# Kernel optimization log

Measured on AMD Instinct MI355X. Metric: run time of the kernel, lower is better.

The kernel has to match this reference:

```python
import jax, jax.numpy as jnp
import numpy as np

D, NH, NL, NP, DFF = 256, 8, 4, 4, 1024
DH = D // NH
SHAPES = [(64, 64), (32, 32), (16, 16), (8, 8)]
LEN = sum(h * w for h, w in SHAPES)  # 5440
B = 4
EPS = 1e-5


def setup_inputs() -> dict:
    key = jax.random.key(0)
    ks = jax.random.split(key, 24)
    def lin_w(k, fin, fout, scale=None):
        s = (1.0 / np.sqrt(fin)) if scale is None else scale
        return jax.random.normal(k, (fin, fout), jnp.float32) * s
    def lin_b(k, fout, scale=0.01):
        return jax.random.normal(k, (fout,), jnp.float32) * scale
    inp = {
        'src': jax.random.normal(ks[0], (B, LEN, D), jnp.float32),
        'pos_lvl_embed': jax.random.normal(ks[1], (B, LEN, D), jnp.float32),
        'spatial_shapes': jnp.array(SHAPES, jnp.int32),
        'level_start_index': jnp.array(np.cumsum([0] + [h * w for h, w in SHAPES[:-1]]), jnp.int32),
        # MSDeformAttn params
        'Wv': lin_w(ks[2], D, D), 'bv': lin_b(ks[3], D),
        'Woff': lin_w(ks[4], D, NH * NL * NP * 2, scale=0.001),  # small offsets, like grid init
        'boff': jax.random.normal(ks[5], (NH * NL * NP * 2,), jnp.float32) * 0.5,
        'Wa': lin_w(ks[6], D, NH * NL * NP), 'ba': lin_b(ks[7], NH * NL * NP),
        'Wo': lin_w(ks[8], D, D), 'bo': lin_b(ks[9], D),
        # FFN params
        'W1': lin_w(ks[10], D, DFF), 'b1': lin_b(ks[11], DFF),
        'W2': lin_w(ks[12], DFF, D), 'b2': lin_b(ks[13], D),
        # LayerNorms
        'g1': jnp.ones((D,), jnp.float32), 'be1': jnp.zeros((D,), jnp.float32),
        'g2': jnp.ones((D,), jnp.float32), 'be2': jnp.zeros((D,), jnp.float32),
    }
    return inp


def _layernorm(x, g, b):
    mu = jnp.mean(x, axis=-1, keepdims=True)
    var = jnp.var(x, axis=-1, keepdims=True)
    return (x - mu) * jax.lax.rsqrt(var + EPS) * g + b


def _bilinear(v, x, y):
    # v: [B, H, W, NH, DH]; x, y: [B, Lq, NH, NP] pixel coords (align_corners=False, zero padding)
    Bv, H, W = v.shape[0], v.shape[1], v.shape[2]
    x0, y0 = jnp.floor(x), jnp.floor(y)
    bb = jnp.arange(Bv)[:, None, None, None]
    hh = jnp.arange(NH)[None, None, :, None]
    out = 0.0
    for dx in (0, 1):
        for dy in (0, 1):
            xi, yi = x0 + dx, y0 + dy
            w = (1.0 - jnp.abs(x - xi)) * (1.0 - jnp.abs(y - yi))
            valid = (xi >= 0) & (xi <= W - 1) & (yi >= 0) & (yi <= H - 1)
            xc = jnp.clip(xi, 0, W - 1).astype(jnp.int32)
            yc = jnp.clip(yi, 0, H - 1).astype(jnp.int32)
            out = out + v[bb, yc, xc, hh] * (w * valid)[..., None]
    return out  # [B, Lq, NH, NP, DH]


def _ms_deform_attn(query, value_flat, shapes, starts, Wv, bv, Woff, boff, Wa, ba, Wo, bo):
    Bq, Lq = query.shape[0], query.shape[1]
    # reference points: normalized center of each query's own spatial location (valid_ratios == 1)
    refs = []
    for (H, W) in shapes:
        gy, gx = jnp.meshgrid(jnp.arange(H, dtype=jnp.float32), jnp.arange(W, dtype=jnp.float32), indexing='ij')
        refs.append(jnp.stack([(gx + 0.5) / W, (gy + 0.5) / H], -1).reshape(-1, 2))
    ref = jnp.concatenate(refs, 0)  # [Len, 2] (x, y)

    value = (value_flat @ Wv + bv).reshape(Bq, Lq, NH, DH)
    off = (query @ Woff + boff).reshape(Bq, Lq, NH, NL, NP, 2)
    attn = jax.nn.softmax((query @ Wa + ba).reshape(Bq, Lq, NH, NL * NP), axis=-1).reshape(Bq, Lq, NH, NL, NP)
    norm = jnp.array([[w, h] for (h, w) in shapes], jnp.float32)  # [NL, 2] = (W, H)
    loc = ref[None, :, None, None, None, :] + off / norm[None, None, None, :, None, :]  # [B,Lq,NH,NL,NP,2]

    out = 0.0
    for l, (H, W) in enumerate(shapes):
        s = starts[l]
        v_l = value[:, s:s + H * W].reshape(Bq, H, W, NH, DH)
        x = loc[:, :, :, l, :, 0] * W - 0.5
        y = loc[:, :, :, l, :, 1] * H - 0.5
        sampled = _bilinear(v_l, x, y)  # [B,Lq,NH,NP,DH]
        out = out + jnp.sum(sampled * attn[:, :, :, l, :, None], axis=3)
    return out.reshape(Bq, Lq, D) @ Wo + bo


def reference(src, spatial_shapes, level_start_index, pos_lvl_embed,
              Wv, bv, Woff, boff, Wa, ba, Wo, bo,
              W1, b1, W2, b2, g1, be1, g2, be2):
    shapes = [(int(h), int(w)) for h, w in np.asarray(spatial_shapes)]  # static metadata
    starts = [int(s) for s in np.asarray(level_start_index)]
    src2 = _ms_deform_attn(src + pos_lvl_embed, src, shapes, starts, Wv, bv, Woff, boff, Wa, ba, Wo, bo)
    x = _layernorm(src + src2, g1, be1)
    ffn = jax.nn.relu(x @ W1 + b1) @ W2 + b2
    return _layernorm(x + ffn, g2, be2)
```

## Files before the change

### kernel.cpp

```cpp
#include <hip/hip_runtime.h>
#include <hip/hip_fp16.h>
#include <cstddef>
#include <cstdint>

#define DMODEL 256
#define NHEAD  8
#define NLVL   4
#define NPT    4
#define DHEAD  32
#define DFFN   1024
#define SLEN   5440
#define BATCH  4
#define NTOK   (BATCH * SLEN)
#define NT256  ((size_t)NTOK * 256)
#define GYR    170
#define GYP    176
#define LN_EPS 1e-5f

typedef __attribute__((ext_vector_type(4))) float f32x4;
typedef __attribute__((ext_vector_type(8))) short s16x8;

__device__ __forceinline__ unsigned short f2bf(float f) {
    union { float f; unsigned u; } v; v.f = f;
    unsigned u = v.u;
    u += 0x7FFFu + ((u >> 16) & 1u);
    return (unsigned short)(u >> 16);
}
__device__ __forceinline__ float bf2f(unsigned short h) {
    union { unsigned u; float f; } v; v.u = ((unsigned)h) << 16;
    return v.f;
}

__device__ __forceinline__ void g2l16(const unsigned short* g, unsigned short* l) {
    __builtin_amdgcn_global_load_lds(
        (const __attribute__((address_space(1))) unsigned int*)g,
        (__attribute__((address_space(3))) unsigned int*)l, 16, 0, 0);
}

__global__ __launch_bounds__(256) void prep_tr_kernel(
    const float* __restrict__ src, const float* __restrict__ pos,
    unsigned short* __restrict__ srcB, unsigned short* __restrict__ qB,
    const float* __restrict__ Wv, const float* __restrict__ Woff,
    const float* __restrict__ Wa, const float* __restrict__ Wo,
    const float* __restrict__ W1, const float* __restrict__ W2,
    unsigned short* __restrict__ WvT, unsigned short* __restrict__ WcatT,
    unsigned short* __restrict__ WoT,
    unsigned short* __restrict__ W1T, unsigned short* __restrict__ W2T)
{
    if (blockIdx.x < 5440) {
        const size_t i = ((size_t)blockIdx.x * 256 + threadIdx.x) * 4;
        const float4 s = *(const float4*)(src + i);
        const float4 p = *(const float4*)(pos + i);
        ushort4 sb, qb;
        sb.x = f2bf(s.x); sb.y = f2bf(s.y); sb.z = f2bf(s.z); sb.w = f2bf(s.w);
        qb.x = f2bf(s.x + p.x); qb.y = f2bf(s.y + p.y);
        qb.z = f2bf(s.z + p.z); qb.w = f2bf(s.w + p.w);
        *(ushort4*)(srcB + i) = sb;
        *(ushort4*)(qB + i) = qb;
        return;
    }
    const int bid = blockIdx.x - 5440;
    const float* W; unsigned short* Wt; int K, N, t;
    if (bid < 16)       { W = Wv;   Wt = WvT;              K = 256;  N = 256;  t = bid; }
    else if (bid < 32)  { W = Woff; Wt = WcatT;            K = 256;  N = 256;  t = bid - 16; }
    else if (bid < 40)  { W = Wa;   Wt = WcatT + 256*256;  K = 256;  N = 128;  t = bid - 32; }
    else if (bid < 56)  { W = Wo;   Wt = WoT;              K = 256;  N = 256;  t = bid - 40; }
    else if (bid < 120) { W = W1;   Wt = W1T;              K = 256;  N = 1024; t = bid - 56; }
    else                { W = W2;   Wt = W2T;              K = 1024; N = 256;  t = bid - 120; }
    const int ntx = N >> 6;
    const int k0 = (t / ntx) * 64, n0 = (t % ntx) * 64;

    __shared__ float T[64][65];
    const int r  = threadIdx.x >> 4;
    const int c4 = (threadIdx.x & 15) * 4;
    #pragma unroll
    for (int rep = 0; rep < 4; rep++) {
        const int k = rep * 16 + r;
        const float4 v = *(const float4*)(W + (size_t)(k0 + k) * N + n0 + c4);
        T[c4 + 0][k] = v.x; T[c4 + 1][k] = v.y;
        T[c4 + 2][k] = v.z; T[c4 + 3][k] = v.w;
    }
    __syncthreads();
    #pragma unroll
    for (int rep = 0; rep < 4; rep++) {
        const int n = rep * 16 + r;
        ushort4 o;
        o.x = f2bf(T[n][c4 + 0]); o.y = f2bf(T[n][c4 + 1]);
        o.z = f2bf(T[n][c4 + 2]); o.w = f2bf(T[n][c4 + 3]);
        *(ushort4*)(Wt + (size_t)(n0 + n) * K + k0 + c4) = o;
    }
}

template <int KK, bool RELU, int OM>
__device__ __forceinline__ void gemm_lds_body(
    const unsigned short* __restrict__ A,
    const unsigned short* __restrict__ Bt,
    const float* __restrict__ bias, const float* __restrict__ bias2,
    int bsplit, void* __restrict__ Cout, int N, int row0, int col0,
    unsigned short (*sA)[8192], unsigned short (*sB)[8192])
{
    const int tid  = threadIdx.x;
    const int wid  = tid >> 6;
    const int lane = tid & 63;
    const int m16  = lane & 15;
    const int q    = lane >> 4;
    const int wr   = (wid >> 1) * 64;
    const int wc   = (wid & 1) * 64;

    const int srow = lane >> 3;
    const int schk = (lane & 7) ^ srow;

    auto stage = [&](int buf, int kt) {
        #pragma unroll
        for (int i = 0; i < 4; i++) {
            const int j = wid * 4 + i;
            const int r = j * 8 + srow;
            g2l16(A  + (size_t)(row0 + r) * KK + kt * 64 + schk * 8,
                  &sA[buf][j * 512]);
            g2l16(Bt + (size_t)(col0 + r) * KK + kt * 64 + schk * 8,
                  &sB[buf][j * 512]);
        }
    };

    f32x4 acc[4][4];
    #pragma unroll
    for (int m = 0; m < 4; m++)
        #pragma unroll
        for (int n = 0; n < 4; n++) acc[m][n] = (f32x4){0.f, 0.f, 0.f, 0.f};

    constexpr int NT = KK / 64;
    stage(0, 0);
    stage(1, 1);

    #pragma unroll 1
    for (int kt = 0; kt < NT; kt++) {
        const int cur = kt & 1;

        if (kt + 1 < NT) asm volatile("s_waitcnt vmcnt(8)" ::: "memory");
        else             asm volatile("s_waitcnt vmcnt(0)" ::: "memory");
        __builtin_amdgcn_sched_barrier(0);
        __builtin_amdgcn_s_barrier();
        __builtin_amdgcn_sched_barrier(0);

        #pragma unroll
        for (int ks = 0; ks < 2; ks++) {
            s16x8 a[4], b[4];
            #pragma unroll
            for (int m = 0; m < 4; m++) {
                const int r  = wr + m * 16 + m16;
                const int cc = (ks * 4 + q) ^ (r & 7);
                a[m] = *(const s16x8*)&sA[cur][r * 64 + cc * 8];
            }
            #pragma unroll
            for (int n = 0; n < 4; n++) {
                const int r  = wc + n * 16 + m16;
                const int cc = (ks * 4 + q) ^ (r & 7);
                b[n] = *(const s16x8*)&sB[cur][r * 64 + cc * 8];
            }
            #pragma unroll
            for (int m = 0; m < 4; m++)
                #pragma unroll
                for (int n = 0; n < 4; n++)
                    acc[m][n] = __builtin_amdgcn_mfma_f32_16x16x32_bf16(
                        a[m], b[n], acc[m][n], 0, 0, 0);
        }

        asm volatile("s_waitcnt lgkmcnt(0)" ::: "memory");
        __builtin_amdgcn_sched_barrier(0);
        __builtin_amdgcn_s_barrier();
        __builtin_amdgcn_sched_barrier(0);

        if (kt + 2 < NT) stage(cur, kt + 2);
    }

    #pragma unroll
    for (int n = 0; n < 4; n++) {
        const int col  = col0 + wc + n * 16 + m16;
        const float bc = (col < bsplit) ? bias[col] : bias2[col - bsplit];
        #pragma unroll
        for (int m = 0; m < 4; m++) {
            #pragma unroll
            for (int r = 0; r < 4; r++) {
                const int row = row0 + wr + m * 16 + q * 4 + r;
                float v = acc[m][n][r] + bc;
                if (RELU) v = fmaxf(v, 0.f);
                if (OM == 1)
                    ((unsigned short*)Cout)[(size_t)row * N + col] = f2bf(v);
                else if (OM == 2)
                    ((__half*)Cout)[(size_t)row * N + col] = __float2half(v);
                else
                    ((float*)Cout)[(size_t)row * N + col] = v;
            }
        }
    }
}

__global__ __launch_bounds__(256, 2) void valolg_kernel(
    const unsigned short* __restrict__ srcB,
    const unsigned short* __restrict__ qB,
    const unsigned short* __restrict__ WvT,
    const unsigned short* __restrict__ WcatT,
    const float* __restrict__ bv, const float* __restrict__ boff,
    const float* __restrict__ ba,
    __half* __restrict__ valB, float* __restrict__ olg)
{
    __shared__ __align__(16) unsigned short sA[2][8192];
    __shared__ __align__(16) unsigned short sB[2][8192];

    if (blockIdx.x < 2 * GYP) {
        const int lin = blockIdx.x;
        const int c8  = lin & 7;
        const int rr  = lin >> 3;
        const int bx  = rr % 2;
        const int yy  = (rr / 2) * 8 + c8;
        if (yy >= GYR) return;
        gemm_lds_body<256, false, 2>(srcB, WvT, bv, bv, 1 << 30,
                                     valB, 256, yy * 128, bx * 128, sA, sB);
    } else {
        const int lin = blockIdx.x - 2 * GYP;
        const int c8  = lin & 7;
        const int rr  = lin >> 3;
        const int bx  = rr % 3;
        const int yy  = (rr / 3) * 8 + c8;
        if (yy >= GYR) return;
        gemm_lds_body<256, false, 0>(qB, WcatT, boff, ba, 256,
                                     olg, 384, yy * 128, bx * 128, sA, sB);
    }
}

__global__ __launch_bounds__(256, 2) void ffn1_kernel(
    const unsigned short* __restrict__ xB,
    const unsigned short* __restrict__ W1T,
    const float* __restrict__ b1, unsigned short* __restrict__ h)
{
    __shared__ __align__(16) unsigned short sA[2][8192];
    __shared__ __align__(16) unsigned short sB[2][8192];
    const int lin = blockIdx.x;
    const int c8  = lin & 7;
    const int rr  = lin >> 3;
    const int bx  = rr % 8;
    const int yy  = (rr / 8) * 8 + c8;
    if (yy >= GYR) return;
    gemm_lds_body<256, true, 1>(xB, W1T, b1, b1, 1 << 30,
                                h, 1024, yy * 128, bx * 128, sA, sB);
}

template <int KK, int LNM>
__global__ __launch_bounds__(256, 2) void gemm64_ln_kernel(
    const unsigned short* __restrict__ A,
    const unsigned short* __restrict__ Bt,
    const float* __restrict__ bias,
    const void* __restrict__ resid,
    const float* __restrict__ g, const float* __restrict__ be,
    void* __restrict__ outp)
{
    const int row0 = blockIdx.x * 64;

    __shared__ __align__(16) unsigned short lds[40960];

    const int tid  = threadIdx.x;
    const int wid  = tid >> 6;
    const int lane = tid & 63;
    const int m16  = lane & 15;
    const int q    = lane >> 4;
    const int wc   = wid * 64;

    const int srow = lane >> 3;
    const int schk = (lane & 7) ^ srow;

    auto stage = [&](int buf, int kt) {
        unsigned short* sAb = lds + buf * 4096;
        unsigned short* sBb = lds + 8192 + buf * 16384;
        #pragma unroll
        for (int i = 0; i < 2; i++) {
            const int j = wid * 2 + i;
            const int r = j * 8 + srow;
            g2l16(A + (size_t)(row0 + r) * KK + kt * 64 + schk * 8,
                  sAb + j * 512);
        }
        #pragma unroll
        for (int i = 0; i < 8; i++) {
            const int j = wid * 8 + i;
            const int r = j * 8 + srow;
            g2l16(Bt + (size_t)r * KK + kt * 64 + schk * 8,
                  sBb + j * 512);
        }
    };

    f32x4 acc[4][4];
    #pragma unroll
    for (int m = 0; m < 4; m++)
        #pragma unroll
        for (int n = 0; n < 4; n++) acc[m][n] = (f32x4){0.f, 0.f, 0.f, 0.f};

    constexpr int NT = KK / 64;
    stage(0, 0);
    stage(1, 1);

    #pragma unroll 1
    for (int kt = 0; kt < NT; kt++) {
        const int cur = kt & 1;
        const unsigned short* sAc = lds + cur * 4096;
        const unsigned short* sBc = lds + 8192 + cur * 16384;

        if (kt + 1 < NT) asm volatile("s_waitcnt vmcnt(10)" ::: "memory");
        else             asm volatile("s_waitcnt vmcnt(0)" ::: "memory");
        __builtin_amdgcn_sched_barrier(0);
        __builtin_amdgcn_s_barrier();
        __builtin_amdgcn_sched_barrier(0);

        #pragma unroll
        for (int ks = 0; ks < 2; ks++) {
            s16x8 a[4], b[4];
            #pragma unroll
            for (int m = 0; m < 4; m++) {
                const int r  = m * 16 + m16;
                const int cc = (ks * 4 + q) ^ (r & 7);
                a[m] = *(const s16x8*)&sAc[r * 64 + cc * 8];
            }
            #pragma unroll
            for (int n = 0; n < 4; n++) {
                const int r  = wc + n * 16 + m16;
                const int cc = (ks * 4 + q) ^ (r & 7);
                b[n] = *(const s16x8*)&sBc[r * 64 + cc * 8];
            }
            #pragma unroll
            for (int m = 0; m < 4; m++)
                #pragma unroll
                for (int n = 0; n < 4; n++)
                    acc[m][n] = __builtin_amdgcn_mfma_f32_16x16x32_bf16(
                        a[m], b[n], acc[m][n], 0, 0, 0);
        }

        asm volatile("s_waitcnt lgkmcnt(0)" ::: "memory");
        __builtin_amdgcn_sched_barrier(0);
        __builtin_amdgcn_s_barrier();
        __builtin_amdgcn_sched_barrier(0);

        if (kt + 2 < NT) stage(cur, kt + 2);
    }
    float* lnbuf = (float*)lds;

    #pragma unroll
    for (int n = 0; n < 4; n++) {
        const int col = wc + n * 16 + m16;
        const float bc = bias[col];
        #pragma unroll
        for (int m = 0; m < 4; m++)
            #pragma unroll
            for (int r = 0; r < 4; r++)
                lnbuf[(m * 16 + q * 4 + r) * 260 + col] = acc[m][n][r] + bc;
    }
    __syncthreads();

    #pragma unroll 1
    for (int rr2 = 0; rr2 < 16; rr2++) {
        const int rl = wid * 16 + rr2;
        const size_t grow = (size_t)row0 + rl;
        const size_t base = grow * 256 + lane * 4;

        float4 v = *(const float4*)&lnbuf[rl * 260 + lane * 4];
        if (LNM == 1) {
            const float4 rv = *(const float4*)((const float*)resid + base);
            v.x += rv.x; v.y += rv.y; v.z += rv.z; v.w += rv.w;
        } else {
            const ushort4 rb = *(const ushort4*)((const unsigned short*)resid + base);
            v.x += bf2f(rb.x); v.y += bf2f(rb.y);
            v.z += bf2f(rb.z); v.w += bf2f(rb.w);
        }

        float s  = v.x + v.y + v.z + v.w;
        float s2 = v.x * v.x + v.y * v.y + v.z * v.z + v.w * v.w;
        #pragma unroll
        for (int o = 32; o > 0; o >>= 1) {
            s  += __shfl_xor(s, o);
            s2 += __shfl_xor(s2, o);
        }
        const float mu  = s * (1.f / 256.f);
        const float var = s2 * (1.f / 256.f) - mu * mu;
        const float rn  = rsqrtf(var + LN_EPS);

        const float4 gv = *(const float4*)(g  + lane * 4);
        const float4 bv = *(const float4*)(be + lane * 4);
        float4 o4;
        o4.x = (v.x - mu) * rn * gv.x + bv.x;
        o4.y = (v.y - mu) * rn * gv.y + bv.y;
        o4.z = (v.z - mu) * rn * gv.z + bv.z;
        o4.w = (v.w - mu) * rn * gv.w + bv.w;
        if (LNM == 1) {
            ushort4 ob;
            ob.x = f2bf(o4.x); ob.y = f2bf(o4.y);
            ob.z = f2bf(o4.z); ob.w = f2bf(o4.w);
            *(ushort4*)((unsigned short*)outp + base) = ob;
        } else {
            *(float4*)((float*)outp + base) = o4;
        }
    }
}

__global__ __launch_bounds__(256) void msda_sample_kernel(
    const __half* __restrict__ value, const float* __restrict__ olg,
    unsigned short* __restrict__ out)
{
    const int lin = blockIdx.x;
    const int c8  = lin & 7;
    const int rr  = lin >> 3;
    const int b   = c8 >> 1;
    const int i8  = (c8 & 1) + 2 * rr;

    const int tid = threadIdx.x;
    const int sub = tid & 3;
    const int h   = (tid >> 2) & 7;
    const int t8  = tid >> 5;
    const int q   = i8 * 8 + t8;
    const int bq  = b * SLEN + q;

    __shared__ __align__(16) uint4 smeta[8 * 16 * 8];

    {
        int rem, Wq;
        if (q < 4096)      { rem = q;        Wq = 64; }
        else if (q < 5120) { rem = q - 4096; Wq = 32; }
        else if (q < 5376) { rem = q - 5120; Wq = 16; }
        else               { rem = q - 5376; Wq = 8;  }
        const int gy = rem / Wq;
        const int gx = rem - gy * Wq;
        const float ref_x = (gx + 0.5f) / (float)Wq;
        const float ref_y = (gy + 0.5f) / (float)Wq;

        const float4 lgv = *(const float4*)(olg + (size_t)bq * 384 + 256 + h * 16 + sub * 4);
        float mx = fmaxf(fmaxf(lgv.x, lgv.y), fmaxf(lgv.z, lgv.w));
        mx = fmaxf(mx, __shfl_xor(mx, 1));
        mx = fmaxf(mx, __shfl_xor(mx, 2));
        float e0 = expf(lgv.x - mx), e1 = expf(lgv.y - mx);
        float e2 = expf(lgv.z - mx), e3 = expf(lgv.w - mx);
        float s = e0 + e1 + e2 + e3;
        s += __shfl_xor(s, 1);
        s += __shfl_xor(s, 2);
        const float inv_s = 1.f / s;

        const float4 o01 = *(const float4*)(olg + (size_t)bq * 384 + h * 32 + sub * 8);
        const float4 o23 = *(const float4*)(olg + (size_t)bq * 384 + h * 32 + sub * 8 + 4);

        constexpr int LW[4] = {64, 32, 16, 8};
        constexpr int LS[4] = {0, 4096, 5120, 5376};
        const int Wl = LW[sub];
        const float fW = (float)Wl;
        const float ew[4] = {e0, e1, e2, e3};
        const float ox[4] = {o01.x, o01.z, o23.x, o23.z};
        const float oy[4] = {o01.y, o01.w, o23.y, o23.w};

        #pragma unroll
        for (int j = 0; j < 4; j++) {
            const float aw = ew[j] * inv_s;
            const float X = (ref_x + ox[j] / fW) * fW - 0.5f;
            const float Y = (ref_y + oy[j] / fW) * fW - 0.5f;
            const float x0f = floorf(X), y0f = floorf(Y);
            const float fx = X - x0f, fy = Y - y0f;
            const int x0 = (int)x0f, y0 = (int)y0f;

            unsigned idx[4]; __half hw[4];
            #pragma unroll
            for (int dy = 0; dy < 2; dy++) {
                const int yi = y0 + dy;
                const float wy = dy ? fy : (1.f - fy);
                const bool vy = (yi >= 0) && (yi < Wl);
                const int yc = min(max(yi, 0), Wl - 1);
                #pragma unroll
                for (int dx = 0; dx < 2; dx++) {
                    const int xi = x0 + dx;
                    const float wx = dx ? fx : (1.f - fx);
                    const bool vx = (xi >= 0) && (xi < Wl);
                    const int xc = min(max(xi, 0), Wl - 1);
                    const int c = dy * 2 + dx;
                    idx[c] = (unsigned)(LS[sub] + yc * Wl + xc);
                    hw[c] = __float2half((vx && vy) ? (aw * wx * wy) : 0.f);
                }
            }
            union { __half2 h2; unsigned u; } pk0, pk1;
            pk0.h2 = __halves2half2(hw[0], hw[1]);
            pk1.h2 = __halves2half2(hw[2], hw[3]);
            uint4 m;
            m.x = idx[0] | (idx[1] << 16);
            m.y = idx[2] | (idx[3] << 16);
            m.z = pk0.u;
            m.w = pk1.u;
            smeta[((t8 * 16) + sub * 4 + j) * 8 + h] = m;
        }
    }
    __syncthreads();

    const char* vb = (const char*)value + (size_t)b * SLEN * 512;
    const unsigned laneoff = (unsigned)(h * 64 + sub * 16);
    const uint4* metap = &smeta[(t8 * 16) * 8 + h];

    __half2 acc[4][4];
    #pragma unroll
    for (int i = 0; i < 4; i++)
        #pragma unroll
        for (int k = 0; k < 4; k++)
            acc[i][k] = __float2half2_rn(0.f);

    for (int g = 0; g < 4; g++) {
        #pragma unroll
        for (int pp = 0; pp < 4; pp++) {
            const int p = g * 4 + pp;
            const uint4 m = metap[p * 8];
            const unsigned a0 = ((m.x & 0xFFFFu) << 9) + laneoff;
            const unsigned a1 = ((m.x >> 16) << 9) + laneoff;
            const unsigned a2 = ((m.y & 0xFFFFu) << 9) + laneoff;
            const unsigned a3 = ((m.y >> 16) << 9) + laneoff;
            const int4 v0 = *(const int4*)(vb + a0);
            const int4 v1 = *(const int4*)(vb + a1);
            const int4 v2 = *(const int4*)(vb + a2);
            const int4 v3 = *(const int4*)(vb + a3);
            union { unsigned u; __half2 h2; } wz, ww;
            wz.u = m.z; ww.u = m.w;
            const __half2 ws0 = __half2half2(__low2half(wz.h2));
            const __half2 ws1 = __half2half2(__high2half(wz.h2));
            const __half2 ws2 = __half2half2(__low2half(ww.h2));
            const __half2 ws3 = __half2half2(__high2half(ww.h2));
            const __half2* p0 = (const __half2*)&v0;
            const __half2* p1 = (const __half2*)&v1;
            const __half2* p2 = (const __half2*)&v2;
            const __half2* p3 = (const __half2*)&v3;
            #pragma unroll
            for (int k = 0; k < 4; k++) {
                acc[pp][k] = __hfma2(ws0, p0[k], acc[pp][k]);
                acc[pp][k] = __hfma2(ws1, p1[k], acc[pp][k]);
                acc[pp][k] = __hfma2(ws2, p2[k], acc[pp][k]);
                acc[pp][k] = __hfma2(ws3, p3[k], acc[pp][k]);
            }
        }
    }

    uint4 o;
    unsigned* ou = &o.x;
    #pragma unroll
    for (int k = 0; k < 4; k++) {
        float2 s = {0.f, 0.f};
        #pragma unroll
        for (int i = 0; i < 4; i++) {
            const float2 f = __half22float2(acc[i][k]);
            s.x += f.x; s.y += f.y;
        }
        ou[k] = (unsigned)f2bf(s.x) | ((unsigned)f2bf(s.y) << 16);
    }
    *(uint4*)(out + (size_t)bq * 256 + h * 32 + sub * 8) = o;
}

extern "C" void kernel_launch(void* const* d_in, const int* in_sizes, int n_in,
                              void* d_out, int out_size, void* d_ws, size_t ws_size,
                              hipStream_t stream)
{
    const float* src  = (const float*)d_in[0];
    const float* pos  = (const float*)d_in[1];
    const float* Wv   = (const float*)d_in[4];
    const float* bv   = (const float*)d_in[5];
    const float* Woff = (const float*)d_in[6];
    const float* boff = (const float*)d_in[7];
    const float* Wa   = (const float*)d_in[8];
    const float* ba   = (const float*)d_in[9];
    const float* Wo   = (const float*)d_in[10];
    const float* bo   = (const float*)d_in[11];
    const float* W1   = (const float*)d_in[12];
    const float* b1   = (const float*)d_in[13];
    const float* W2   = (const float*)d_in[14];
    const float* b2   = (const float*)d_in[15];
    const float* g1   = (const float*)d_in[16];
    const float* be1  = (const float*)d_in[17];
    const float* g2   = (const float*)d_in[18];
    const float* be2  = (const float*)d_in[19];
    float* out = (float*)d_out;

    char* wsp = (char*)d_ws;
    unsigned short* srcB = (unsigned short*)wsp; wsp += NT256 * 2;
    unsigned short* qB   = (unsigned short*)wsp; wsp += NT256 * 2;
    __half*         valB = (__half*)wsp;         wsp += NT256 * 2;
    float*          olg  = (float*)wsp;          wsp += (size_t)NTOK * 384 * 4;
    unsigned short* aoB  = (unsigned short*)wsp; wsp += NT256 * 2;
    unsigned short* xB   = (unsigned short*)wsp; wsp += NT256 * 2;
    unsigned short* h    = (unsigned short*)wsp; wsp += (size_t)NTOK * 1024 * 2;
    unsigned short* WvT  = (unsigned short*)wsp; wsp += 256 * 256 * 2;
    unsigned short* WcatT= (unsigned short*)wsp; wsp += 384 * 256 * 2;
    unsigned short* WoT  = (unsigned short*)wsp; wsp += 256 * 256 * 2;
    unsigned short* W1T  = (unsigned short*)wsp; wsp += 1024 * 256 * 2;
    unsigned short* W2T  = (unsigned short*)wsp; wsp += 256 * 1024 * 2;

    const dim3 blk(256);

    prep_tr_kernel<<<dim3(5624), blk, 0, stream>>>(
        src, pos, srcB, qB, Wv, Woff, Wa, Wo, W1, W2,
        WvT, WcatT, WoT, W1T, W2T);

    valolg_kernel<<<dim3(5 * GYP), blk, 0, stream>>>(
        srcB, qB, WvT, WcatT, bv, boff, ba, valB, olg);

    msda_sample_kernel<<<dim3(NTOK / 8), blk, 0, stream>>>(valB, olg, aoB);

    gemm64_ln_kernel<256, 1><<<dim3(NTOK / 64), blk, 0, stream>>>(
        aoB, WoT, bo, src, g1, be1, xB);

    ffn1_kernel<<<dim3(8 * GYP), blk, 0, stream>>>(xB, W1T, b1, h);

    gemm64_ln_kernel<1024, 2><<<dim3(NTOK / 64), blk, 0, stream>>>(
        h, W2T, b2, xB, g2, be2, out);
}
```

Measured before the change: 238.4 us.

## Fuse fp32-to-bf16 input conversion and pos add into value/offset GEMM loads

Removes the elementwise prep pass that wrote bf16 copies of src and src+pos. The value and offset/attention GEMM now read the fp32 inputs directly, add pos where needed, convert to bf16 in registers and store the A tile into LDS. The cost removed is one kernel's worth of round-trip global traffic for two bf16 activation buffers. In exchange, the A tiles are no longer loaded asynchronously and are single-buffered. The fp32 reads are twice as wide, src is re-read by every column tile, and pos is re-read by the 3 olg column tiles.

Result: no change. 239.5 us (median of 2 runs) (+0.5%).

```diff
diff --git a/kernel.cpp b/kernel.cpp
--- a/kernel.cpp
+++ b/kernel.cpp
@@ -37,9 +37,7 @@
         (__attribute__((address_space(3))) unsigned int*)l, 16, 0, 0);
 }
 
-__global__ __launch_bounds__(256) void prep_tr_kernel(
-    const float* __restrict__ src, const float* __restrict__ pos,
-    unsigned short* __restrict__ srcB, unsigned short* __restrict__ qB,
+__global__ __launch_bounds__(256) void tr_kernel(
     const float* __restrict__ Wv, const float* __restrict__ Woff,
     const float* __restrict__ Wa, const float* __restrict__ Wo,
     const float* __restrict__ W1, const float* __restrict__ W2,
@@ -47,19 +45,7 @@
     unsigned short* __restrict__ WoT,
     unsigned short* __restrict__ W1T, unsigned short* __restrict__ W2T)
 {
-    if (blockIdx.x < 5440) {
-        const size_t i = ((size_t)blockIdx.x * 256 + threadIdx.x) * 4;
-        const float4 s = *(const float4*)(src + i);
-        const float4 p = *(const float4*)(pos + i);
-        ushort4 sb, qb;
-        sb.x = f2bf(s.x); sb.y = f2bf(s.y); sb.z = f2bf(s.z); sb.w = f2bf(s.w);
-        qb.x = f2bf(s.x + p.x); qb.y = f2bf(s.y + p.y);
-        qb.z = f2bf(s.z + p.z); qb.w = f2bf(s.w + p.w);
-        *(ushort4*)(srcB + i) = sb;
-        *(ushort4*)(qB + i) = qb;
-        return;
-    }
-    const int bid = blockIdx.x - 5440;
+    const int bid = blockIdx.x;
     const float* W; unsigned short* Wt; int K, N, t;
     if (bid < 16)       { W = Wv;   Wt = WvT;              K = 256;  N = 256;  t = bid; }
     else if (bid < 32)  { W = Woff; Wt = WcatT;            K = 256;  N = 256;  t = bid - 16; }
@@ -88,6 +74,135 @@
         o.x = f2bf(T[n][c4 + 0]); o.y = f2bf(T[n][c4 + 1]);
         o.z = f2bf(T[n][c4 + 2]); o.w = f2bf(T[n][c4 + 3]);
         *(ushort4*)(Wt + (size_t)(n0 + n) * K + k0 + c4) = o;
+    }
+}
+
+template <int ASRC, int OM>
+__device__ __forceinline__ void gemm_prep_body(
+    const float* __restrict__ srcf, const float* __restrict__ posf,
+    const unsigned short* __restrict__ Bt,
+    const float* __restrict__ bias, const float* __restrict__ bias2,
+    int bsplit, void* __restrict__ Cout, int N, int row0, int col0,
+    unsigned short* sA, unsigned short* sB)
+{
+    const int tid  = threadIdx.x;
+    const int wid  = tid >> 6;
+    const int lane = tid & 63;
+    const int m16  = lane & 15;
+    const int q    = lane >> 4;
+    const int wr   = (wid >> 1) * 64;
+    const int wc   = (wid & 1) * 64;
+    const int srow = lane >> 3;
+    const int schk = (lane & 7) ^ srow;
+
+    f32x4 acc[4][4];
+    #pragma unroll
+    for (int m = 0; m < 4; m++)
+        #pragma unroll
+        for (int n = 0; n < 4; n++) acc[m][n] = (f32x4){0.f, 0.f, 0.f, 0.f};
+
+    #pragma unroll 1
+    for (int kt = 0; kt < 4; kt++) {
+        #pragma unroll
+        for (int i = 0; i < 4; i++) {
+            const int j = wid * 4 + i;
+            const int r = j * 8 + srow;
+            const size_t go = (size_t)(row0 + r) * 256 + kt * 64 + schk * 8;
+            const float4 f0 = *(const float4*)(srcf + go);
+            const float4 f1 = *(const float4*)(srcf + go + 4);
+            s16x8 av;
+            if (ASRC) {
+                const float4 p0 = *(const float4*)(posf + go);
+                const float4 p1 = *(const float4*)(posf + go + 4);
+                av[0] = (short)f2bf(f0.x + p0.x); av[1] = (short)f2bf(f0.y + p0.y);
+                av[2] = (short)f2bf(f0.z + p0.z); av[3] = (short)f2bf(f0.w + p0.w);
+                av[4] = (short)f2bf(f1.x + p1.x); av[5] = (short)f2bf(f1.y + p1.y);
+                av[6] = (short)f2bf(f1.z + p1.z); av[7] = (short)f2bf(f1.w + p1.w);
+            } else {
+                av[0] = (short)f2bf(f0.x); av[1] = (short)f2bf(f0.y);
+                av[2] = (short)f2bf(f0.z); av[3] = (short)f2bf(f0.w);
+                av[4] = (short)f2bf(f1.x); av[5] = (short)f2bf(f1.y);
+                av[6] = (short)f2bf(f1.z); av[7] = (short)f2bf(f1.w);
+            }
+            *(s16x8*)&sA[j * 512 + lane * 8] = av;
+            g2l16(Bt + (size_t)(col0 + r) * 256 + kt * 64 + schk * 8,
+                  sB + j * 512);
+        }
+        __syncthreads();
+
+        #pragma unroll
+        for (int ks = 0; ks < 2; ks++) {
+            s16x8 a[4], b[4];
+            #pragma unroll
+            for (int m = 0; m < 4; m++) {
+                const int r  = wr + m * 16 + m16;
+                const int cc = (ks * 4 + q) ^ (r & 7);
+                a[m] = *(const s16x8*)&sA[r * 64 + cc * 8];
+            }
+            #pragma unroll
+            for (int n = 0; n < 4; n++) {
+                const int r  = wc + n * 16 + m16;
+                const int cc = (ks * 4 + q) ^ (r & 7);
+                b[n] = *(const s16x8*)&sB[r * 64 + cc * 8];
+            }
+            #pragma unroll
+            for (int m = 0; m < 4; m++)
+                #pragma unroll
+                for (int n = 0; n < 4; n++)
+                    acc[m][n] = __builtin_amdgcn_mfma_f32_16x16x32_bf16(
+                        a[m], b[n], acc[m][n], 0, 0, 0);
+        }
+        __syncthreads();
+    }
+
+    #pragma unroll
+    for (int n = 0; n < 4; n++) {
+        const int col  = col0 + wc + n * 16 + m16;
+        const float bc = (col < bsplit) ? bias[col] : bias2[col - bsplit];
+        #pragma unroll
+        for (int m = 0; m < 4; m++) {
+            #pragma unroll
+            for (int r = 0; r < 4; r++) {
+                const int row = row0 + wr + m * 16 + q * 4 + r;
+                float v = acc[m][n][r] + bc;
+                if (OM == 2)
+                    ((__half*)Cout)[(size_t)row * N + col] = __float2half(v);
+                else
+                    ((float*)Cout)[(size_t)row * N + col] = v;
+            }
+        }
+    }
+}
+
+__global__ __launch_bounds__(256, 2) void valolg_kernel(
+    const float* __restrict__ src, const float* __restrict__ pos,
+    const unsigned short* __restrict__ WvT,
+    const unsigned short* __restrict__ WcatT,
+    const float* __restrict__ bv, const float* __restrict__ boff,
+    const float* __restrict__ ba,
+    __half* __restrict__ valB, float* __restrict__ olg)
+{
+    __shared__ __align__(16) unsigned short sA[8192];
+    __shared__ __align__(16) unsigned short sB[8192];
+
+    if (blockIdx.x < 2 * GYP) {
+        const int lin = blockIdx.x;
+        const int c8  = lin & 7;
+        const int rr  = lin >> 3;
+        const int bx  = rr % 2;
+        const int yy  = (rr / 2) * 8 + c8;
+        if (yy >= GYR) return;
+        gemm_prep_body<0, 2>(src, pos, WvT, bv, bv, 1 << 30,
+                             valB, 256, yy * 128, bx * 128, sA, sB);
+    } else {
+        const int lin = blockIdx.x - 2 * GYP;
+        const int c8  = lin & 7;
+        const int rr  = lin >> 3;
+        const int bx  = rr % 3;
+        const int yy  = (rr / 3) * 8 + c8;
+        if (yy >= GYR) return;
+        gemm_prep_body<1, 0>(src, pos, WcatT, boff, ba, 256,
+                             olg, 384, yy * 128, bx * 128, sA, sB);
     }
 }
 
@@ -192,39 +307,6 @@
                     ((float*)Cout)[(size_t)row * N + col] = v;
             }
         }
-    }
-}
-
-__global__ __launch_bounds__(256, 2) void valolg_kernel(
-    const unsigned short* __restrict__ srcB,
-    const unsigned short* __restrict__ qB,
-    const unsigned short* __restrict__ WvT,
-    const unsigned short* __restrict__ WcatT,
-    const float* __restrict__ bv, const float* __restrict__ boff,
-    const float* __restrict__ ba,
-    __half* __restrict__ valB, float* __restrict__ olg)
-{
-    __shared__ __align__(16) unsigned short sA[2][8192];
-    __shared__ __align__(16) unsigned short sB[2][8192];
-
-    if (blockIdx.x < 2 * GYP) {
-        const int lin = blockIdx.x;
-        const int c8  = lin & 7;
-        const int rr  = lin >> 3;
-        const int bx  = rr % 2;
-        const int yy  = (rr / 2) * 8 + c8;
-        if (yy >= GYR) return;
-        gemm_lds_body<256, false, 2>(srcB, WvT, bv, bv, 1 << 30,
-                                     valB, 256, yy * 128, bx * 128, sA, sB);
-    } else {
-        const int lin = blockIdx.x - 2 * GYP;
-        const int c8  = lin & 7;
-        const int rr  = lin >> 3;
-        const int bx  = rr % 3;
-        const int yy  = (rr / 3) * 8 + c8;
-        if (yy >= GYR) return;
-        gemm_lds_body<256, false, 0>(qB, WcatT, boff, ba, 256,
-                                     olg, 384, yy * 128, bx * 128, sA, sB);
     }
 }
 
@@ -574,8 +656,6 @@
     float* out = (float*)d_out;
 
     char* wsp = (char*)d_ws;
-    unsigned short* srcB = (unsigned short*)wsp; wsp += NT256 * 2;
-    unsigned short* qB   = (unsigned short*)wsp; wsp += NT256 * 2;
     __half*         valB = (__half*)wsp;         wsp += NT256 * 2;
     float*          olg  = (float*)wsp;          wsp += (size_t)NTOK * 384 * 4;
     unsigned short* aoB  = (unsigned short*)wsp; wsp += NT256 * 2;
@@ -589,12 +669,11 @@
 
     const dim3 blk(256);
 
-    prep_tr_kernel<<<dim3(5624), blk, 0, stream>>>(
-        src, pos, srcB, qB, Wv, Woff, Wa, Wo, W1, W2,
-        WvT, WcatT, WoT, W1T, W2T);
+    tr_kernel<<<dim3(184), blk, 0, stream>>>(
+        Wv, Woff, Wa, Wo, W1, W2, WvT, WcatT, WoT, W1T, W2T);
 
     valolg_kernel<<<dim3(5 * GYP), blk, 0, stream>>>(
-        srcB, qB, WvT, WcatT, bv, boff, ba, valB, olg);
+        src, pos, WvT, WcatT, bv, boff, ba, valB, olg);
 
     msda_sample_kernel<<<dim3(NTOK / 8), blk, 0, stream>>>(valB, olg, aoB);
 
```
